# Kernel tuning notes

Measured on AMD Instinct MI355X. Metric: run time of the kernel, lower is better.

Reference implementation:

```python
import jax, jax.numpy as jnp
import numpy as np

B, C, IC, H, W = 2, 64, 32, 96, 96


def setup_inputs() -> dict:
    key = jax.random.key(0)
    ks = jax.random.split(key, 8)
    s_in = 1.0 / np.sqrt(C)
    s_ic = 1.0 / np.sqrt(IC)
    return {
        "x": jax.random.normal(ks[0], (B, C, H, W), dtype=jnp.float32),
        "Wg": jax.random.uniform(ks[1], (IC, C), jnp.float32, -s_in, s_in),
        "bg": jax.random.uniform(ks[2], (IC,), jnp.float32, -s_in, s_in),
        "Wt": jax.random.uniform(ks[3], (IC, C), jnp.float32, -s_in, s_in),
        "bt": jax.random.uniform(ks[4], (IC,), jnp.float32, -s_in, s_in),
        "Wp": jax.random.uniform(ks[5], (IC, C), jnp.float32, -s_in, s_in),
        "bp": jax.random.uniform(ks[6], (IC,), jnp.float32, -s_in, s_in),
        "Wo": jax.random.uniform(ks[7], (C, IC), jnp.float32, -s_ic, s_ic),
        "bo": jax.random.uniform(jax.random.fold_in(key, 9), (C,), jnp.float32, -s_ic, s_ic),
    }


def reference(x, Wg, bg, Wt, bt, Wp, bp, Wo, bo):
    b, c, h, w = x.shape
    n = h * w
    xf = x.reshape(b, c, n)  # [B, C, N]

    def proj(Wc, bc):  # 1x1 conv == channel GEMM -> [B, IC, N]
        return jnp.einsum("bcn,oc->bon", xf, Wc) + bc[None, :, None]

    g = proj(Wg, bg)
    theta = proj(Wt, bt)
    phi = proj(Wp, bp)
    scores = jnp.einsum("bcn,bcm->bnm", theta, phi)  # [B, N, N]
    att = jax.nn.softmax(scores, axis=-1)
    y = jnp.einsum("bnm,bcm->bcn", att, g)  # [B, IC, N]
    o = jnp.einsum("bcn,oc->bon", y, Wo) + bo[None, :, None]  # [B, C, N]
    return o.reshape(b, c, h, w) + x
```

## Files before the change

### kernel.cpp

```cpp
#include <hip/hip_runtime.h>
#include <hip/hip_bf16.h>


#define B_   2
#define C_   64
#define IC_  32
#define N_   9216
#define QBLK128    72
#define LOG2E 1.44269504088896f

typedef __attribute__((ext_vector_type(4))) float  f32x4;
typedef __attribute__((ext_vector_type(8))) short  s16x8;
typedef __attribute__((ext_vector_type(4))) short  s16x4;

static __device__ __forceinline__ ushort f2bf(float f) {
  union { __hip_bfloat16 h; ushort u; } cv;
  cv.h = __float2bfloat16(f);
  return cv.u;
}

static __device__ __forceinline__ float bf2f(ushort u) {
  union { uint i; float f; } c;
  c.i = ((uint)u) << 16;
  return c.f;
}

static __device__ __forceinline__ f32x4 mfma32(s16x8 a, s16x8 b, f32x4 c) {
  return __builtin_amdgcn_mfma_f32_16x16x32_bf16(a, b, c, 0, 0, 0);
}

__global__ __launch_bounds__(256) void proj_kernel(
    const float* __restrict__ x,
    const float* __restrict__ Wg, const float* __restrict__ bg,
    const float* __restrict__ Wt, const float* __restrict__ bt,
    const float* __restrict__ Wp, const float* __restrict__ bp,
    ushort* __restrict__ Qb, ushort* __restrict__ Kb, ushort* __restrict__ Vt)
{
  const int grp = blockIdx.x / 72;
  const int ic0 = grp * 8;
  const int bn  = (blockIdx.x % 72) * 256 + threadIdx.x;
  const int b   = bn / N_;
  const int n   = bn % N_;

  float ag[8], at_[8], ap[8];
#pragma unroll
  for (int j = 0; j < 8; ++j) { ag[j] = 0.f; at_[j] = 0.f; ap[j] = 0.f; }

  const float* xp = x + (size_t)b * C_ * N_ + n;
#pragma unroll 8
  for (int c = 0; c < C_; ++c) {
    const float xv = xp[(size_t)c * N_];
#pragma unroll
    for (int j = 0; j < 8; ++j) {
      ag[j]  = fmaf(Wg[(ic0 + j) * C_ + c], xv, ag[j]);
      at_[j] = fmaf(Wt[(ic0 + j) * C_ + c], xv, at_[j]);
      ap[j]  = fmaf(Wp[(ic0 + j) * C_ + c], xv, ap[j]);
    }
  }

  union { ushort u[8]; s16x8 v; } qv, kv;
#pragma unroll
  for (int j = 0; j < 8; ++j) {
    const int ic = ic0 + j;
    qv.u[j] = f2bf(LOG2E * (at_[j] + bt[ic]));
    kv.u[j] = f2bf(ap[j] + bp[ic]);
  }
  *reinterpret_cast<s16x8*>(Qb + (size_t)bn * IC_ + ic0) = qv.v;
  *reinterpret_cast<s16x8*>(Kb + (size_t)bn * IC_ + ic0) = kv.v;

  const int j6 = n & 63, u = j6 >> 5, r = j6 & 31;
  const int nperm = (n - j6) + u * 32 + (r & 15) * 2 + (r >> 4);
#pragma unroll
  for (int j = 0; j < 8; ++j) {
    const int ic = ic0 + j;
    Vt[(size_t)(b * IC_ + ic) * N_ + nperm] = f2bf(ag[j] + bg[ic]);
  }
}

template<int NSEG>
__global__ __launch_bounds__(256, 4) void attn_kernel(
    const ushort* __restrict__ Qb, const ushort* __restrict__ Kb,
    const ushort* __restrict__ Vt, ushort* __restrict__ Opart,
    float* __restrict__ Lp)
{
  constexpr int NT = 144 / NSEG;
  constexpr int SKEYS = N_ / NSEG;
  constexpr int KSTR = 36;
  constexpr int VSTR = 70;
  __shared__ __align__(16) ushort Kl[64 * KSTR];
  __shared__ __align__(16) ushort Vl[32 * VSTR];

  const int qblk = blockIdx.x % QBLK128;
  const int bs   = blockIdx.x / QBLK128;
  const int seg  = bs % NSEG;
  const int b    = bs / NSEG;
  const int key0 = seg * SKEYS;

  const int tid  = threadIdx.x;
  const int lane = tid & 63;
  const int wave = tid >> 6;
  const int q16  = lane & 15;
  const int h    = lane >> 4;

  const int qbaseA = qblk * 128 + wave * 32;
  const int qbaseB = qbaseA + 16;

  const short ONE = (short)0x3F80;
  const s16x8 ones = {ONE, ONE, ONE, ONE, ONE, ONE, ONE, ONE};

  const s16x8 qfragA = *reinterpret_cast<const s16x8*>(
      Qb + (size_t)(b * N_ + qbaseA + q16) * IC_ + h * 8);
  const s16x8 qfragB = *reinterpret_cast<const s16x8*>(
      Qb + (size_t)(b * N_ + qbaseB + q16) * IC_ + h * 8);

  f32x4 aA0 = {0.f,0.f,0.f,0.f}, aA1 = {0.f,0.f,0.f,0.f}, aLA = {0.f,0.f,0.f,0.f};
  f32x4 aB0 = {0.f,0.f,0.f,0.f}, aB1 = {0.f,0.f,0.f,0.f}, aLB = {0.f,0.f,0.f,0.f};

  const int krow = tid >> 2, kpart = tid & 3;
  const ushort* kg = Kb + ((size_t)b * N_ + key0 + krow) * IC_ + kpart * 8;
  ushort* kl_dst = &Kl[krow * KSTR + kpart * 8];

  const int vd = tid >> 3, vp = tid & 7;
  const ushort* vg = Vt + (size_t)(b * IC_ + vd) * N_ + key0 + vp * 8;
  ushort* vl_dst = &Vl[vd * VSTR + vp * 8];

  s16x8 kreg = *reinterpret_cast<const s16x8*>(kg);
  s16x8 vreg = *reinterpret_cast<const s16x8*>(vg);

  for (int it = 0; it < NT; ++it) {
    *reinterpret_cast<s16x8*>(kl_dst) = kreg;
    *reinterpret_cast<s16x8*>(vl_dst) = vreg;
    __syncthreads();

    if (it + 1 < NT) {
      kg += 64 * IC_;
      vg += 64;
      kreg = *reinterpret_cast<const s16x8*>(kg);
      vreg = *reinterpret_cast<const s16x8*>(vg);
    }

    const s16x8 kf00 = *reinterpret_cast<const s16x8*>(&Kl[(q16)      * KSTR + h * 8]);
    const s16x8 kf01 = *reinterpret_cast<const s16x8*>(&Kl[(16 + q16) * KSTR + h * 8]);
    const s16x8 kf10 = *reinterpret_cast<const s16x8*>(&Kl[(32 + q16) * KSTR + h * 8]);
    const s16x8 kf11 = *reinterpret_cast<const s16x8*>(&Kl[(48 + q16) * KSTR + h * 8]);
    const f32x4 z = {0.f, 0.f, 0.f, 0.f};
    __builtin_amdgcn_s_setprio(1);
    const f32x4 sA0 = mfma32(kf00, qfragA, z);
    const f32x4 sA1 = mfma32(kf01, qfragA, z);
    const f32x4 sB0 = mfma32(kf00, qfragB, z);
    const f32x4 sB1 = mfma32(kf01, qfragB, z);
    const f32x4 sA2 = mfma32(kf10, qfragA, z);
    const f32x4 sA3 = mfma32(kf11, qfragA, z);
    const f32x4 sB2 = mfma32(kf10, qfragB, z);
    const f32x4 sB3 = mfma32(kf11, qfragB, z);
    __builtin_amdgcn_s_setprio(0);

    union { ushort us[8]; s16x8 v; } paA0, paA1, paB0, paB1;
#pragma unroll
    for (int i = 0; i < 4; ++i) {
      paA0.us[2 * i]     = f2bf(__builtin_amdgcn_exp2f(sA0[i]));
      paA0.us[2 * i + 1] = f2bf(__builtin_amdgcn_exp2f(sA1[i]));
      paA1.us[2 * i]     = f2bf(__builtin_amdgcn_exp2f(sA2[i]));
      paA1.us[2 * i + 1] = f2bf(__builtin_amdgcn_exp2f(sA3[i]));
      paB0.us[2 * i]     = f2bf(__builtin_amdgcn_exp2f(sB0[i]));
      paB0.us[2 * i + 1] = f2bf(__builtin_amdgcn_exp2f(sB1[i]));
      paB1.us[2 * i]     = f2bf(__builtin_amdgcn_exp2f(sB2[i]));
      paB1.us[2 * i + 1] = f2bf(__builtin_amdgcn_exp2f(sB3[i]));
    }

    const s16x8 vf00 = *reinterpret_cast<const s16x8*>(&Vl[q16 * VSTR + h * 8]);
    const s16x8 vf01 = *reinterpret_cast<const s16x8*>(&Vl[(16 + q16) * VSTR + h * 8]);
    const s16x8 vf10 = *reinterpret_cast<const s16x8*>(&Vl[q16 * VSTR + 32 + h * 8]);
    const s16x8 vf11 = *reinterpret_cast<const s16x8*>(&Vl[(16 + q16) * VSTR + 32 + h * 8]);
    __builtin_amdgcn_s_setprio(1);
    aA0 = mfma32(paA0.v, vf00, aA0);
    aA1 = mfma32(paA0.v, vf01, aA1);
    aB0 = mfma32(paB0.v, vf00, aB0);
    aB1 = mfma32(paB0.v, vf01, aB1);
    aA0 = mfma32(paA1.v, vf10, aA0);
    aA1 = mfma32(paA1.v, vf11, aA1);
    aB0 = mfma32(paB1.v, vf10, aB0);
    aB1 = mfma32(paB1.v, vf11, aB1);
    aLA = mfma32(paA0.v, ones, aLA);
    aLA = mfma32(paA1.v, ones, aLA);
    aLB = mfma32(paB0.v, ones, aLB);
    aLB = mfma32(paB1.v, ones, aLB);
    __builtin_amdgcn_s_setprio(0);
    __syncthreads();
  }

  const size_t obase0 = ((size_t)(b * NSEG + seg) * N_);
#pragma unroll
  for (int r = 0; r < 4; ++r) {
    const int qA = qbaseA + h * 4 + r;
    const int qB = qbaseB + h * 4 + r;
    Opart[(obase0 + qA) * IC_ + q16]      = f2bf(aA0[r]);
    Opart[(obase0 + qA) * IC_ + 16 + q16] = f2bf(aA1[r]);
    Opart[(obase0 + qB) * IC_ + q16]      = f2bf(aB0[r]);
    Opart[(obase0 + qB) * IC_ + 16 + q16] = f2bf(aB1[r]);
  }
  if (q16 == 0) {
#pragma unroll
    for (int r = 0; r < 4; ++r) {
      Lp[obase0 + qbaseA + h * 4 + r] = aLA[r];
      Lp[obase0 + qbaseB + h * 4 + r] = aLB[r];
    }
  }
}

template<int NSEG>
__global__ __launch_bounds__(256) void combine_kernel(
    const ushort* __restrict__ Opart, const float* __restrict__ Lp,
    ushort* __restrict__ Y)
{
  const int idx = blockIdx.x * 256 + threadIdx.x;
  const int bn  = idx >> 3;
  const int e   = idx & 7;
  const int b   = bn / N_;
  const int q   = bn % N_;

  float l = 0.f;
  float o[4];
#pragma unroll
  for (int j = 0; j < 4; ++j) o[j] = 0.f;

#pragma unroll
  for (int s = 0; s < NSEG; ++s) {
    const size_t base = (size_t)(b * NSEG + s) * N_ + q;
    l += Lp[base];
    union { s16x4 v; ushort us[4]; } ov;
    ov.v = *reinterpret_cast<const s16x4*>(Opart + base * IC_ + e * 4);
#pragma unroll
    for (int j = 0; j < 4; ++j) o[j] += bf2f(ov.us[j]);
  }
  const float inv = 1.0f / l;
  union { ushort us[4]; s16x4 v; } yv;
#pragma unroll
  for (int j = 0; j < 4; ++j) yv.us[j] = f2bf(o[j] * inv);
  *reinterpret_cast<s16x4*>(Y + (size_t)bn * IC_ + e * 4) = yv.v;
}

__global__ __launch_bounds__(256) void out_kernel(
    const ushort* __restrict__ Y, const float* __restrict__ Wo,
    const float* __restrict__ bo, const float* __restrict__ x,
    float* __restrict__ out)
{
  const int g    = blockIdx.x / 72;
  const int oc0  = g * 8;
  const int bn   = (blockIdx.x % 72) * 256 + threadIdx.x;
  const int b    = bn / N_;
  const int n    = bn % N_;

  float yv[32];
#pragma unroll
  for (int i = 0; i < 4; ++i) {
    union { s16x8 v; ushort us[8]; } ov;
    ov.v = *reinterpret_cast<const s16x8*>(Y + (size_t)bn * IC_ + i * 8);
#pragma unroll
    for (int j = 0; j < 8; ++j) yv[i * 8 + j] = bf2f(ov.us[j]);
  }

  float acc[8];
#pragma unroll
  for (int j = 0; j < 8; ++j) acc[j] = bo[oc0 + j];

#pragma unroll
  for (int ic = 0; ic < IC_; ++ic) {
    const float yv_ic = yv[ic];
#pragma unroll
    for (int j = 0; j < 8; ++j)
      acc[j] = fmaf(Wo[(oc0 + j) * IC_ + ic], yv_ic, acc[j]);
  }

#pragma unroll
  for (int j = 0; j < 8; ++j) {
    const int oc = oc0 + j;
    const size_t xi = (size_t)(b * C_ + oc) * N_ + n;
    out[xi] = acc[j] + x[xi];
  }
}

extern "C" void kernel_launch(void* const* d_in, const int* in_sizes, int n_in,
                              void* d_out, int out_size, void* d_ws, size_t ws_size,
                              hipStream_t stream)
{
  const float* x  = (const float*)d_in[0];
  const float* Wg = (const float*)d_in[1];
  const float* bg = (const float*)d_in[2];
  const float* Wt = (const float*)d_in[3];
  const float* bt = (const float*)d_in[4];
  const float* Wp = (const float*)d_in[5];
  const float* bp = (const float*)d_in[6];
  const float* Wo = (const float*)d_in[7];
  const float* bo = (const float*)d_in[8];
  float* out = (float*)d_out;

  char* ws = (char*)d_ws;
  const size_t szb = (size_t)B_ * N_ * IC_ * sizeof(ushort);
  ushort* Qb = (ushort*)(ws);
  ushort* Kb = (ushort*)(ws + szb);
  ushort* Vt = (ushort*)(ws + 2 * szb);
  ushort* Op = (ushort*)(ws + 3 * szb);
  ushort* Yb = (ushort*)(ws);

  const size_t need16 = 3 * szb + 16 * szb + (size_t)16 * B_ * N_ * sizeof(float);

  proj_kernel<<<288, 256, 0, stream>>>(x, Wg, bg, Wt, bt, Wp, bp, Qb, Kb, Vt);
  if (ws_size >= need16) {
    float* Lp = (float*)(ws + 3 * szb + 16 * szb);
    attn_kernel<16><<<B_ * 16 * QBLK128, 256, 0, stream>>>(Qb, Kb, Vt, Op, Lp);
    combine_kernel<16><<<(B_ * N_ * 8) / 256, 256, 0, stream>>>(Op, Lp, Yb);
  } else {
    float* Lp = (float*)(ws + 3 * szb + 8 * szb);
    attn_kernel<8><<<B_ * 8 * QBLK128, 256, 0, stream>>>(Qb, Kb, Vt, Op, Lp);
    combine_kernel<8><<<(B_ * N_ * 8) / 256, 256, 0, stream>>>(Op, Lp, Yb);
  }
  out_kernel<<<8 * 72, 256, 0, stream>>>(Yb, Wo, bo, x, out);
}
```

Baseline: 75.57 us.

## Load K/V fragments directly from global, remap blocks, fuse combine with output projection

The attention kernel drops its LDS staging and both barriers, so each wave loads its K and V MFMA fragments straight from global memory (relying on L2/L1 for reuse across waves and blocks). Block indices are also remapped in an XCD-aware interleaved way so that blocks sharing the same K/V segment land on the same XCD. The separate combine and output-projection kernels are merged into one epilogue kernel, which removes the Y round trip and one launch. The cost is more global/cache traffic per wave, uncoalesced fragment loads, and a heavier per-thread epilogue with 32 accumulators and only 72 blocks.

```diff
diff --git a/kernel.cpp b/kernel.cpp
--- a/kernel.cpp
+++ b/kernel.cpp
@@ -85,13 +85,13 @@
 {
   constexpr int NT = 144 / NSEG;
   constexpr int SKEYS = N_ / NSEG;
-  constexpr int KSTR = 36;
-  constexpr int VSTR = 70;
-  __shared__ __align__(16) ushort Kl[64 * KSTR];
-  __shared__ __align__(16) ushort Vl[32 * VSTR];
-
-  const int qblk = blockIdx.x % QBLK128;
-  const int bs   = blockIdx.x / QBLK128;
+
+  constexpr int NWG = B_ * NSEG * QBLK128;
+  const int bid = blockIdx.x;
+  const int wg  = (bid & 7) * (NWG >> 3) + (bid >> 3);
+
+  const int qblk = wg % QBLK128;
+  const int bs   = wg / QBLK128;
   const int seg  = bs % NSEG;
   const int b    = bs / NSEG;
   const int key0 = seg * SKEYS;
@@ -116,33 +116,21 @@
   f32x4 aA0 = {0.f,0.f,0.f,0.f}, aA1 = {0.f,0.f,0.f,0.f}, aLA = {0.f,0.f,0.f,0.f};
   f32x4 aB0 = {0.f,0.f,0.f,0.f}, aB1 = {0.f,0.f,0.f,0.f}, aLB = {0.f,0.f,0.f,0.f};
 
-  const int krow = tid >> 2, kpart = tid & 3;
-  const ushort* kg = Kb + ((size_t)b * N_ + key0 + krow) * IC_ + kpart * 8;
-  ushort* kl_dst = &Kl[krow * KSTR + kpart * 8];
-
-  const int vd = tid >> 3, vp = tid & 7;
-  const ushort* vg = Vt + (size_t)(b * IC_ + vd) * N_ + key0 + vp * 8;
-  ushort* vl_dst = &Vl[vd * VSTR + vp * 8];
-
-  s16x8 kreg = *reinterpret_cast<const s16x8*>(kg);
-  s16x8 vreg = *reinterpret_cast<const s16x8*>(vg);
+  const ushort* kp  = Kb + ((size_t)b * N_ + key0 + q16) * IC_ + h * 8;
+  const ushort* vp0 = Vt + ((size_t)(b * IC_ + q16)) * N_ + key0 + h * 8;
+  const ushort* vp1 = Vt + ((size_t)(b * IC_ + 16 + q16)) * N_ + key0 + h * 8;
 
   for (int it = 0; it < NT; ++it) {
-    *reinterpret_cast<s16x8*>(kl_dst) = kreg;
-    *reinterpret_cast<s16x8*>(vl_dst) = vreg;
-    __syncthreads();
-
-    if (it + 1 < NT) {
-      kg += 64 * IC_;
-      vg += 64;
-      kreg = *reinterpret_cast<const s16x8*>(kg);
-      vreg = *reinterpret_cast<const s16x8*>(vg);
-    }
-
-    const s16x8 kf00 = *reinterpret_cast<const s16x8*>(&Kl[(q16)      * KSTR + h * 8]);
-    const s16x8 kf01 = *reinterpret_cast<const s16x8*>(&Kl[(16 + q16) * KSTR + h * 8]);
-    const s16x8 kf10 = *reinterpret_cast<const s16x8*>(&Kl[(32 + q16) * KSTR + h * 8]);
-    const s16x8 kf11 = *reinterpret_cast<const s16x8*>(&Kl[(48 + q16) * KSTR + h * 8]);
+    const s16x8 kf00 = *reinterpret_cast<const s16x8*>(kp);
+    const s16x8 kf01 = *reinterpret_cast<const s16x8*>(kp + 16 * IC_);
+    const s16x8 kf10 = *reinterpret_cast<const s16x8*>(kp + 32 * IC_);
+    const s16x8 kf11 = *reinterpret_cast<const s16x8*>(kp + 48 * IC_);
+    const s16x8 vf00 = *reinterpret_cast<const s16x8*>(vp0);
+    const s16x8 vf01 = *reinterpret_cast<const s16x8*>(vp1);
+    const s16x8 vf10 = *reinterpret_cast<const s16x8*>(vp0 + 32);
+    const s16x8 vf11 = *reinterpret_cast<const s16x8*>(vp1 + 32);
+    kp += 64 * IC_; vp0 += 64; vp1 += 64;
+
     const f32x4 z = {0.f, 0.f, 0.f, 0.f};
     __builtin_amdgcn_s_setprio(1);
     const f32x4 sA0 = mfma32(kf00, qfragA, z);
@@ -168,10 +156,6 @@
       paB1.us[2 * i + 1] = f2bf(__builtin_amdgcn_exp2f(sB3[i]));
     }
 
-    const s16x8 vf00 = *reinterpret_cast<const s16x8*>(&Vl[q16 * VSTR + h * 8]);
-    const s16x8 vf01 = *reinterpret_cast<const s16x8*>(&Vl[(16 + q16) * VSTR + h * 8]);
-    const s16x8 vf10 = *reinterpret_cast<const s16x8*>(&Vl[q16 * VSTR + 32 + h * 8]);
-    const s16x8 vf11 = *reinterpret_cast<const s16x8*>(&Vl[(16 + q16) * VSTR + 32 + h * 8]);
     __builtin_amdgcn_s_setprio(1);
     aA0 = mfma32(paA0.v, vf00, aA0);
     aA1 = mfma32(paA0.v, vf01, aA1);
@@ -186,7 +170,6 @@
     aLB = mfma32(paB0.v, ones, aLB);
     aLB = mfma32(paB1.v, ones, aLB);
     __builtin_amdgcn_s_setprio(0);
-    __syncthreads();
   }
 
   const size_t obase0 = ((size_t)(b * NSEG + seg) * N_);
@@ -209,74 +192,53 @@
 }
 
 template<int NSEG>
-__global__ __launch_bounds__(256) void combine_kernel(
+__global__ __launch_bounds__(256) void epilogue_kernel(
     const ushort* __restrict__ Opart, const float* __restrict__ Lp,
-    ushort* __restrict__ Y)
-{
-  const int idx = blockIdx.x * 256 + threadIdx.x;
-  const int bn  = idx >> 3;
-  const int e   = idx & 7;
-  const int b   = bn / N_;
-  const int q   = bn % N_;
+    const float* __restrict__ Wo, const float* __restrict__ bo,
+    const float* __restrict__ x, float* __restrict__ out)
+{
+  const int bn = blockIdx.x * 256 + threadIdx.x;
+  const int b  = bn / N_;
+  const int n  = bn % N_;
 
   float l = 0.f;
-  float o[4];
-#pragma unroll
-  for (int j = 0; j < 4; ++j) o[j] = 0.f;
-
-#pragma unroll
+  float y[32];
+#pragma unroll
+  for (int j = 0; j < 32; ++j) y[j] = 0.f;
+
   for (int s = 0; s < NSEG; ++s) {
-    const size_t base = (size_t)(b * NSEG + s) * N_ + q;
+    const size_t base = (size_t)(b * NSEG + s) * N_ + n;
     l += Lp[base];
-    union { s16x4 v; ushort us[4]; } ov;
-    ov.v = *reinterpret_cast<const s16x4*>(Opart + base * IC_ + e * 4);
-#pragma unroll
-    for (int j = 0; j < 4; ++j) o[j] += bf2f(ov.us[j]);
+#pragma unroll
+    for (int i = 0; i < 4; ++i) {
+      union { s16x8 v; ushort us[8]; } ov;
+      ov.v = *reinterpret_cast<const s16x8*>(Opart + base * IC_ + i * 8);
+#pragma unroll
+      for (int j = 0; j < 8; ++j) y[i * 8 + j] += bf2f(ov.us[j]);
+    }
   }
   const float inv = 1.0f / l;
-  union { ushort us[4]; s16x4 v; } yv;
-#pragma unroll
-  for (int j = 0; j < 4; ++j) yv.us[j] = f2bf(o[j] * inv);
-  *reinterpret_cast<s16x4*>(Y + (size_t)bn * IC_ + e * 4) = yv.v;
-}
-
-__global__ __launch_bounds__(256) void out_kernel(
-    const ushort* __restrict__ Y, const float* __restrict__ Wo,
-    const float* __restrict__ bo, const float* __restrict__ x,
-    float* __restrict__ out)
-{
-  const int g    = blockIdx.x / 72;
-  const int oc0  = g * 8;
-  const int bn   = (blockIdx.x % 72) * 256 + threadIdx.x;
-  const int b    = bn / N_;
-  const int n    = bn % N_;
-
-  float yv[32];
-#pragma unroll
-  for (int i = 0; i < 4; ++i) {
-    union { s16x8 v; ushort us[8]; } ov;
-    ov.v = *reinterpret_cast<const s16x8*>(Y + (size_t)bn * IC_ + i * 8);
-#pragma unroll
-    for (int j = 0; j < 8; ++j) yv[i * 8 + j] = bf2f(ov.us[j]);
-  }
-
-  float acc[8];
-#pragma unroll
-  for (int j = 0; j < 8; ++j) acc[j] = bo[oc0 + j];
-
-#pragma unroll
-  for (int ic = 0; ic < IC_; ++ic) {
-    const float yv_ic = yv[ic];
-#pragma unroll
-    for (int j = 0; j < 8; ++j)
-      acc[j] = fmaf(Wo[(oc0 + j) * IC_ + ic], yv_ic, acc[j]);
-  }
-
-#pragma unroll
-  for (int j = 0; j < 8; ++j) {
-    const int oc = oc0 + j;
-    const size_t xi = (size_t)(b * C_ + oc) * N_ + n;
-    out[xi] = acc[j] + x[xi];
+#pragma unroll
+  for (int j = 0; j < 32; ++j) y[j] *= inv;
+
+#pragma unroll
+  for (int p = 0; p < 4; ++p) {
+    float acc[16];
+#pragma unroll
+    for (int j = 0; j < 16; ++j) acc[j] = bo[p * 16 + j];
+#pragma unroll
+    for (int ic = 0; ic < IC_; ++ic) {
+      const float yv = y[ic];
+#pragma unroll
+      for (int j = 0; j < 16; ++j)
+        acc[j] = fmaf(Wo[(p * 16 + j) * IC_ + ic], yv, acc[j]);
+    }
+#pragma unroll
+    for (int j = 0; j < 16; ++j) {
+      const int oc = p * 16 + j;
+      const size_t xi = (size_t)(b * C_ + oc) * N_ + n;
+      out[xi] = acc[j] + x[xi];
+    }
   }
 }
 
@@ -301,7 +263,6 @@
   ushort* Kb = (ushort*)(ws + szb);
   ushort* Vt = (ushort*)(ws + 2 * szb);
   ushort* Op = (ushort*)(ws + 3 * szb);
-  ushort* Yb = (ushort*)(ws);
 
   const size_t need16 = 3 * szb + 16 * szb + (size_t)16 * B_ * N_ * sizeof(float);
 
@@ -309,11 +270,10 @@
   if (ws_size >= need16) {
     float* Lp = (float*)(ws + 3 * szb + 16 * szb);
     attn_kernel<16><<<B_ * 16 * QBLK128, 256, 0, stream>>>(Qb, Kb, Vt, Op, Lp);
-    combine_kernel<16><<<(B_ * N_ * 8) / 256, 256, 0, stream>>>(Op, Lp, Yb);
+    epilogue_kernel<16><<<(B_ * N_) / 256, 256, 0, stream>>>(Op, Lp, Wo, bo, x, out);
   } else {
     float* Lp = (float*)(ws + 3 * szb + 8 * szb);
     attn_kernel<8><<<B_ * 8 * QBLK128, 256, 0, stream>>>(Qb, Kb, Vt, Op, Lp);
-    combine_kernel<8><<<(B_ * N_ * 8) / 256, 256, 0, stream>>>(Op, Lp, Yb);
-  }
-  out_kernel<<<8 * 72, 256, 0, stream>>>(Yb, Wo, bo, x, out);
-}
+    epilogue_kernel<8><<<(B_ * N_) / 256, 256, 0, stream>>>(Op, Lp, Wo, bo, x, out);
+  }
+}
```

New measurement: 115.5 us. 52.8% more time.

## Widen attention query tile to 64 per wave, add 24-way key split

Applied to the files above, without the earlier changes.

Each wave now handles 64 queries in four 16-row groups instead of 32, so every K/V tile staged in shared memory serves twice as many queries. The loop is restructured to interleave score MFMA, exp and PV MFMA per group, which keeps fewer score registers live at once. A 24-segment key split is added when the workspace is large enough, restoring grid size. The output projection kernel drops to 4 output channels per thread with twice the blocks. The cost is more accumulator registers, which may lower occupancy, and more partial results for the combine step to read.

```diff
diff --git a/kernel.cpp b/kernel.cpp
--- a/kernel.cpp
+++ b/kernel.cpp
@@ -6,7 +6,6 @@
 #define C_   64
 #define IC_  32
 #define N_   9216
-#define QBLK128    72
 #define LOG2E 1.44269504088896f
 
 typedef __attribute__((ext_vector_type(4))) float  f32x4;
@@ -85,13 +84,14 @@
 {
   constexpr int NT = 144 / NSEG;
   constexpr int SKEYS = N_ / NSEG;
+  constexpr int QBLK = N_ / 256;
   constexpr int KSTR = 36;
   constexpr int VSTR = 70;
   __shared__ __align__(16) ushort Kl[64 * KSTR];
   __shared__ __align__(16) ushort Vl[32 * VSTR];
 
-  const int qblk = blockIdx.x % QBLK128;
-  const int bs   = blockIdx.x / QBLK128;
+  const int qblk = blockIdx.x % QBLK;
+  const int bs   = blockIdx.x / QBLK;
   const int seg  = bs % NSEG;
   const int b    = bs / NSEG;
   const int key0 = seg * SKEYS;
@@ -102,27 +102,29 @@
   const int q16  = lane & 15;
   const int h    = lane >> 4;
 
-  const int qbaseA = qblk * 128 + wave * 32;
-  const int qbaseB = qbaseA + 16;
+  const int qbase = qblk * 256 + wave * 64;
 
   const short ONE = (short)0x3F80;
   const s16x8 ones = {ONE, ONE, ONE, ONE, ONE, ONE, ONE, ONE};
 
-  const s16x8 qfragA = *reinterpret_cast<const s16x8*>(
-      Qb + (size_t)(b * N_ + qbaseA + q16) * IC_ + h * 8);
-  const s16x8 qfragB = *reinterpret_cast<const s16x8*>(
-      Qb + (size_t)(b * N_ + qbaseB + q16) * IC_ + h * 8);
+  const ushort* qptr = Qb + (size_t)(b * N_ + qbase + q16) * IC_ + h * 8;
+  const s16x8 qfA = *reinterpret_cast<const s16x8*>(qptr);
+  const s16x8 qfB = *reinterpret_cast<const s16x8*>(qptr + 16 * IC_);
+  const s16x8 qfC = *reinterpret_cast<const s16x8*>(qptr + 32 * IC_);
+  const s16x8 qfD = *reinterpret_cast<const s16x8*>(qptr + 48 * IC_);
 
   f32x4 aA0 = {0.f,0.f,0.f,0.f}, aA1 = {0.f,0.f,0.f,0.f}, aLA = {0.f,0.f,0.f,0.f};
   f32x4 aB0 = {0.f,0.f,0.f,0.f}, aB1 = {0.f,0.f,0.f,0.f}, aLB = {0.f,0.f,0.f,0.f};
+  f32x4 aC0 = {0.f,0.f,0.f,0.f}, aC1 = {0.f,0.f,0.f,0.f}, aLC = {0.f,0.f,0.f,0.f};
+  f32x4 aD0 = {0.f,0.f,0.f,0.f}, aD1 = {0.f,0.f,0.f,0.f}, aLD = {0.f,0.f,0.f,0.f};
 
   const int krow = tid >> 2, kpart = tid & 3;
   const ushort* kg = Kb + ((size_t)b * N_ + key0 + krow) * IC_ + kpart * 8;
   ushort* kl_dst = &Kl[krow * KSTR + kpart * 8];
 
-  const int vd = tid >> 3, vp = tid & 7;
-  const ushort* vg = Vt + (size_t)(b * IC_ + vd) * N_ + key0 + vp * 8;
-  ushort* vl_dst = &Vl[vd * VSTR + vp * 8];
+  const int vd = tid >> 3, vpp = tid & 7;
+  const ushort* vg = Vt + (size_t)(b * IC_ + vd) * N_ + key0 + vpp * 8;
+  ushort* vl_dst = &Vl[vd * VSTR + vpp * 8];
 
   s16x8 kreg = *reinterpret_cast<const s16x8*>(kg);
   s16x8 vreg = *reinterpret_cast<const s16x8*>(vg);
@@ -139,71 +141,106 @@
       vreg = *reinterpret_cast<const s16x8*>(vg);
     }
 
-    const s16x8 kf00 = *reinterpret_cast<const s16x8*>(&Kl[(q16)      * KSTR + h * 8]);
-    const s16x8 kf01 = *reinterpret_cast<const s16x8*>(&Kl[(16 + q16) * KSTR + h * 8]);
-    const s16x8 kf10 = *reinterpret_cast<const s16x8*>(&Kl[(32 + q16) * KSTR + h * 8]);
-    const s16x8 kf11 = *reinterpret_cast<const s16x8*>(&Kl[(48 + q16) * KSTR + h * 8]);
-    const f32x4 z = {0.f, 0.f, 0.f, 0.f};
-    __builtin_amdgcn_s_setprio(1);
-    const f32x4 sA0 = mfma32(kf00, qfragA, z);
-    const f32x4 sA1 = mfma32(kf01, qfragA, z);
-    const f32x4 sB0 = mfma32(kf00, qfragB, z);
-    const f32x4 sB1 = mfma32(kf01, qfragB, z);
-    const f32x4 sA2 = mfma32(kf10, qfragA, z);
-    const f32x4 sA3 = mfma32(kf11, qfragA, z);
-    const f32x4 sB2 = mfma32(kf10, qfragB, z);
-    const f32x4 sB3 = mfma32(kf11, qfragB, z);
-    __builtin_amdgcn_s_setprio(0);
-
-    union { ushort us[8]; s16x8 v; } paA0, paA1, paB0, paB1;
-#pragma unroll
-    for (int i = 0; i < 4; ++i) {
-      paA0.us[2 * i]     = f2bf(__builtin_amdgcn_exp2f(sA0[i]));
-      paA0.us[2 * i + 1] = f2bf(__builtin_amdgcn_exp2f(sA1[i]));
-      paA1.us[2 * i]     = f2bf(__builtin_amdgcn_exp2f(sA2[i]));
-      paA1.us[2 * i + 1] = f2bf(__builtin_amdgcn_exp2f(sA3[i]));
-      paB0.us[2 * i]     = f2bf(__builtin_amdgcn_exp2f(sB0[i]));
-      paB0.us[2 * i + 1] = f2bf(__builtin_amdgcn_exp2f(sB1[i]));
-      paB1.us[2 * i]     = f2bf(__builtin_amdgcn_exp2f(sB2[i]));
-      paB1.us[2 * i + 1] = f2bf(__builtin_amdgcn_exp2f(sB3[i]));
+#pragma unroll
+    for (int u = 0; u < 2; ++u) {
+      const s16x8 kf0 = *reinterpret_cast<const s16x8*>(&Kl[(u * 32 + q16) * KSTR + h * 8]);
+      const s16x8 kf1 = *reinterpret_cast<const s16x8*>(&Kl[(u * 32 + 16 + q16) * KSTR + h * 8]);
+      const s16x8 vf0 = *reinterpret_cast<const s16x8*>(&Vl[q16 * VSTR + u * 32 + h * 8]);
+      const s16x8 vf1 = *reinterpret_cast<const s16x8*>(&Vl[(16 + q16) * VSTR + u * 32 + h * 8]);
+      const f32x4 z = {0.f, 0.f, 0.f, 0.f};
+
+      {
+        __builtin_amdgcn_s_setprio(1);
+        const f32x4 s0 = mfma32(kf0, qfA, z);
+        const f32x4 s1 = mfma32(kf1, qfA, z);
+        __builtin_amdgcn_s_setprio(0);
+        union { ushort us[8]; s16x8 v; } pa;
+#pragma unroll
+        for (int i = 0; i < 4; ++i) {
+          pa.us[2 * i]     = f2bf(__builtin_amdgcn_exp2f(s0[i]));
+          pa.us[2 * i + 1] = f2bf(__builtin_amdgcn_exp2f(s1[i]));
+        }
+        __builtin_amdgcn_s_setprio(1);
+        aA0 = mfma32(pa.v, vf0, aA0);
+        aA1 = mfma32(pa.v, vf1, aA1);
+        aLA = mfma32(pa.v, ones, aLA);
+        __builtin_amdgcn_s_setprio(0);
+      }
+      {
+        __builtin_amdgcn_s_setprio(1);
+        const f32x4 s0 = mfma32(kf0, qfB, z);
+        const f32x4 s1 = mfma32(kf1, qfB, z);
+        __builtin_amdgcn_s_setprio(0);
+        union { ushort us[8]; s16x8 v; } pa;
+#pragma unroll
+        for (int i = 0; i < 4; ++i) {
+          pa.us[2 * i]     = f2bf(__builtin_amdgcn_exp2f(s0[i]));
+          pa.us[2 * i + 1] = f2bf(__builtin_amdgcn_exp2f(s1[i]));
+        }
+        __builtin_amdgcn_s_setprio(1);
+        aB0 = mfma32(pa.v, vf0, aB0);
+        aB1 = mfma32(pa.v, vf1, aB1);
+        aLB = mfma32(pa.v, ones, aLB);
+        __builtin_amdgcn_s_setprio(0);
+      }
+      {
+        __builtin_amdgcn_s_setprio(1);
+        const f32x4 s0 = mfma32(kf0, qfC, z);
+        const f32x4 s1 = mfma32(kf1, qfC, z);
+        __builtin_amdgcn_s_setprio(0);
+        union { ushort us[8]; s16x8 v; } pa;
+#pragma unroll
+        for (int i = 0; i < 4; ++i) {
+          pa.us[2 * i]     = f2bf(__builtin_amdgcn_exp2f(s0[i]));
+          pa.us[2 * i + 1] = f2bf(__builtin_amdgcn_exp2f(s1[i]));
+        }
+        __builtin_amdgcn_s_setprio(1);
+        aC0 = mfma32(pa.v, vf0, aC0);
+        aC1 = mfma32(pa.v, vf1, aC1);
+        aLC = mfma32(pa.v, ones, aLC);
+        __builtin_amdgcn_s_setprio(0);
+      }
+      {
+        __builtin_amdgcn_s_setprio(1);
+        const f32x4 s0 = mfma32(kf0, qfD, z);
+        const f32x4 s1 = mfma32(kf1, qfD, z);
+        __builtin_amdgcn_s_setprio(0);
+        union { ushort us[8]; s16x8 v; } pa;
+#pragma unroll
+        for (int i = 0; i < 4; ++i) {
+          pa.us[2 * i]     = f2bf(__builtin_amdgcn_exp2f(s0[i]));
+          pa.us[2 * i + 1] = f2bf(__builtin_amdgcn_exp2f(s1[i]));
+        }
+        __builtin_amdgcn_s_setprio(1);
+        aD0 = mfma32(pa.v, vf0, aD0);
+        aD1 = mfma32(pa.v, vf1, aD1);
+        aLD = mfma32(pa.v, ones, aLD);
+        __builtin_amdgcn_s_setprio(0);
+      }
     }
-
-    const s16x8 vf00 = *reinterpret_cast<const s16x8*>(&Vl[q16 * VSTR + h * 8]);
-    const s16x8 vf01 = *reinterpret_cast<const s16x8*>(&Vl[(16 + q16) * VSTR + h * 8]);
-    const s16x8 vf10 = *reinterpret_cast<const s16x8*>(&Vl[q16 * VSTR + 32 + h * 8]);
-    const s16x8 vf11 = *reinterpret_cast<const s16x8*>(&Vl[(16 + q16) * VSTR + 32 + h * 8]);
-    __builtin_amdgcn_s_setprio(1);
-    aA0 = mfma32(paA0.v, vf00, aA0);
-    aA1 = mfma32(paA0.v, vf01, aA1);
-    aB0 = mfma32(paB0.v, vf00, aB0);
-    aB1 = mfma32(paB0.v, vf01, aB1);
-    aA0 = mfma32(paA1.v, vf10, aA0);
-    aA1 = mfma32(paA1.v, vf11, aA1);
-    aB0 = mfma32(paB1.v, vf10, aB0);
-    aB1 = mfma32(paB1.v, vf11, aB1);
-    aLA = mfma32(paA0.v, ones, aLA);
-    aLA = mfma32(paA1.v, ones, aLA);
-    aLB = mfma32(paB0.v, ones, aLB);
-    aLB = mfma32(paB1.v, ones, aLB);
-    __builtin_amdgcn_s_setprio(0);
     __syncthreads();
   }
 
   const size_t obase0 = ((size_t)(b * NSEG + seg) * N_);
 #pragma unroll
   for (int r = 0; r < 4; ++r) {
-    const int qA = qbaseA + h * 4 + r;
-    const int qB = qbaseB + h * 4 + r;
-    Opart[(obase0 + qA) * IC_ + q16]      = f2bf(aA0[r]);
-    Opart[(obase0 + qA) * IC_ + 16 + q16] = f2bf(aA1[r]);
-    Opart[(obase0 + qB) * IC_ + q16]      = f2bf(aB0[r]);
-    Opart[(obase0 + qB) * IC_ + 16 + q16] = f2bf(aB1[r]);
+    const int qA = qbase + h * 4 + r;
+    Opart[(obase0 + qA) * IC_ + q16]           = f2bf(aA0[r]);
+    Opart[(obase0 + qA) * IC_ + 16 + q16]      = f2bf(aA1[r]);
+    Opart[(obase0 + qA + 16) * IC_ + q16]      = f2bf(aB0[r]);
+    Opart[(obase0 + qA + 16) * IC_ + 16 + q16] = f2bf(aB1[r]);
+    Opart[(obase0 + qA + 32) * IC_ + q16]      = f2bf(aC0[r]);
+    Opart[(obase0 + qA + 32) * IC_ + 16 + q16] = f2bf(aC1[r]);
+    Opart[(obase0 + qA + 48) * IC_ + q16]      = f2bf(aD0[r]);
+    Opart[(obase0 + qA + 48) * IC_ + 16 + q16] = f2bf(aD1[r]);
   }
   if (q16 == 0) {
 #pragma unroll
     for (int r = 0; r < 4; ++r) {
-      Lp[obase0 + qbaseA + h * 4 + r] = aLA[r];
-      Lp[obase0 + qbaseB + h * 4 + r] = aLB[r];
+      Lp[obase0 + qbase + h * 4 + r]      = aLA[r];
+      Lp[obase0 + qbase + 16 + h * 4 + r] = aLB[r];
+      Lp[obase0 + qbase + 32 + h * 4 + r] = aLC[r];
+      Lp[obase0 + qbase + 48 + h * 4 + r] = aLD[r];
     }
   }
 }
@@ -246,7 +283,7 @@
     float* __restrict__ out)
 {
   const int g    = blockIdx.x / 72;
-  const int oc0  = g * 8;
+  const int oc0  = g * 4;
   const int bn   = (blockIdx.x % 72) * 256 + threadIdx.x;
   const int b    = bn / N_;
   const int n    = bn % N_;
@@ -260,20 +297,20 @@
     for (int j = 0; j < 8; ++j) yv[i * 8 + j] = bf2f(ov.us[j]);
   }
 
-  float acc[8];
-#pragma unroll
-  for (int j = 0; j < 8; ++j) acc[j] = bo[oc0 + j];
+  float acc[4];
+#pragma unroll
+  for (int j = 0; j < 4; ++j) acc[j] = bo[oc0 + j];
 
 #pragma unroll
   for (int ic = 0; ic < IC_; ++ic) {
     const float yv_ic = yv[ic];
 #pragma unroll
-    for (int j = 0; j < 8; ++j)
+    for (int j = 0; j < 4; ++j)
       acc[j] = fmaf(Wo[(oc0 + j) * IC_ + ic], yv_ic, acc[j]);
   }
 
 #pragma unroll
-  for (int j = 0; j < 8; ++j) {
+  for (int j = 0; j < 4; ++j) {
     const int oc = oc0 + j;
     const size_t xi = (size_t)(b * C_ + oc) * N_ + n;
     out[xi] = acc[j] + x[xi];
@@ -303,17 +340,22 @@
   ushort* Op = (ushort*)(ws + 3 * szb);
   ushort* Yb = (ushort*)(ws);
 
+  const size_t need24 = 3 * szb + 24 * szb + (size_t)24 * B_ * N_ * sizeof(float);
   const size_t need16 = 3 * szb + 16 * szb + (size_t)16 * B_ * N_ * sizeof(float);
 
   proj_kernel<<<288, 256, 0, stream>>>(x, Wg, bg, Wt, bt, Wp, bp, Qb, Kb, Vt);
-  if (ws_size >= need16) {
+  if (ws_size >= need24) {
+    float* Lp = (float*)(ws + 3 * szb + 24 * szb);
+    attn_kernel<24><<<B_ * 24 * (N_ / 256), 256, 0, stream>>>(Qb, Kb, Vt, Op, Lp);
+    combine_kernel<24><<<(B_ * N_ * 8) / 256, 256, 0, stream>>>(Op, Lp, Yb);
+  } else if (ws_size >= need16) {
     float* Lp = (float*)(ws + 3 * szb + 16 * szb);
-    attn_kernel<16><<<B_ * 16 * QBLK128, 256, 0, stream>>>(Qb, Kb, Vt, Op, Lp);
+    attn_kernel<16><<<B_ * 16 * (N_ / 256), 256, 0, stream>>>(Qb, Kb, Vt, Op, Lp);
     combine_kernel<16><<<(B_ * N_ * 8) / 256, 256, 0, stream>>>(Op, Lp, Yb);
   } else {
     float* Lp = (float*)(ws + 3 * szb + 8 * szb);
-    attn_kernel<8><<<B_ * 8 * QBLK128, 256, 0, stream>>>(Qb, Kb, Vt, Op, Lp);
+    attn_kernel<8><<<B_ * 8 * (N_ / 256), 256, 0, stream>>>(Qb, Kb, Vt, Op, Lp);
     combine_kernel<8><<<(B_ * N_ * 8) / 256, 256, 0, stream>>>(Op, Lp, Yb);
   }
-  out_kernel<<<8 * 72, 256, 0, stream>>>(Yb, Wo, bo, x, out);
-}
+  out_kernel<<<16 * 72, 256, 0, stream>>>(Yb, Wo, bo, x, out);
+}
```

Measured after the change: 69.78 us. 7.7% less time.

## Fuse split-KV combine with output projection and raise attention occupancy bound

Applied to the files above, without the earlier changes.

Merges the combine kernel (summing partial attention outputs and normalising) with the output 1x1 projection plus residual into one epilogue kernel. Normalised rows are staged in LDS, so the Y buffer no longer makes a bf16 round trip through global memory and one launch is removed. Also raises the attention kernel's launch_bounds min-blocks from 4 to 8, which pressures the compiler to cap registers per thread and may cause spills. The epilogue uses 32 positions per block, so each block does one x/out store per channel strip, which may coalesce less well than before.

```diff
diff --git a/kernel.cpp b/kernel.cpp
--- a/kernel.cpp
+++ b/kernel.cpp
@@ -6,7 +6,7 @@
 #define C_   64
 #define IC_  32
 #define N_   9216
-#define QBLK128    72
+#define QBLK128 72
 #define LOG2E 1.44269504088896f
 
 typedef __attribute__((ext_vector_type(4))) float  f32x4;
@@ -78,7 +78,7 @@
 }
 
 template<int NSEG>
-__global__ __launch_bounds__(256, 4) void attn_kernel(
+__global__ __launch_bounds__(256, 8) void attn_kernel(
     const ushort* __restrict__ Qb, const ushort* __restrict__ Kb,
     const ushort* __restrict__ Vt, ushort* __restrict__ Opart,
     float* __restrict__ Lp)
@@ -120,9 +120,9 @@
   const ushort* kg = Kb + ((size_t)b * N_ + key0 + krow) * IC_ + kpart * 8;
   ushort* kl_dst = &Kl[krow * KSTR + kpart * 8];
 
-  const int vd = tid >> 3, vp = tid & 7;
-  const ushort* vg = Vt + (size_t)(b * IC_ + vd) * N_ + key0 + vp * 8;
-  ushort* vl_dst = &Vl[vd * VSTR + vp * 8];
+  const int vd = tid >> 3, vpp = tid & 7;
+  const ushort* vg = Vt + (size_t)(b * IC_ + vd) * N_ + key0 + vpp * 8;
+  ushort* vl_dst = &Vl[vd * VSTR + vpp * 8];
 
   s16x8 kreg = *reinterpret_cast<const s16x8*>(kg);
   s16x8 vreg = *reinterpret_cast<const s16x8*>(vg);
@@ -209,74 +209,66 @@
 }
 
 template<int NSEG>
-__global__ __launch_bounds__(256) void combine_kernel(
+__global__ __launch_bounds__(256) void epilogue_kernel(
     const ushort* __restrict__ Opart, const float* __restrict__ Lp,
-    ushort* __restrict__ Y)
+    const float* __restrict__ Wo, const float* __restrict__ bo,
+    const float* __restrict__ x, float* __restrict__ out)
 {
-  const int idx = blockIdx.x * 256 + threadIdx.x;
-  const int bn  = idx >> 3;
-  const int e   = idx & 7;
-  const int b   = bn / N_;
-  const int q   = bn % N_;
-
-  float l = 0.f;
-  float o[4];
-#pragma unroll
-  for (int j = 0; j < 4; ++j) o[j] = 0.f;
-
-#pragma unroll
-  for (int s = 0; s < NSEG; ++s) {
-    const size_t base = (size_t)(b * NSEG + s) * N_ + q;
-    l += Lp[base];
-    union { s16x4 v; ushort us[4]; } ov;
-    ov.v = *reinterpret_cast<const s16x4*>(Opart + base * IC_ + e * 4);
-#pragma unroll
-    for (int j = 0; j < 4; ++j) o[j] += bf2f(ov.us[j]);
-  }
-  const float inv = 1.0f / l;
-  union { ushort us[4]; s16x4 v; } yv;
-#pragma unroll
-  for (int j = 0; j < 4; ++j) yv.us[j] = f2bf(o[j] * inv);
-  *reinterpret_cast<s16x4*>(Y + (size_t)bn * IC_ + e * 4) = yv.v;
-}
-
-__global__ __launch_bounds__(256) void out_kernel(
-    const ushort* __restrict__ Y, const float* __restrict__ Wo,
-    const float* __restrict__ bo, const float* __restrict__ x,
-    float* __restrict__ out)
-{
-  const int g    = blockIdx.x / 72;
-  const int oc0  = g * 8;
-  const int bn   = (blockIdx.x % 72) * 256 + threadIdx.x;
-  const int b    = bn / N_;
-  const int n    = bn % N_;
-
-  float yv[32];
-#pragma unroll
-  for (int i = 0; i < 4; ++i) {
-    union { s16x8 v; ushort us[8]; } ov;
-    ov.v = *reinterpret_cast<const s16x8*>(Y + (size_t)bn * IC_ + i * 8);
-#pragma unroll
-    for (int j = 0; j < 8; ++j) yv[i * 8 + j] = bf2f(ov.us[j]);
-  }
-
-  float acc[8];
-#pragma unroll
-  for (int j = 0; j < 8; ++j) acc[j] = bo[oc0 + j];
-
-#pragma unroll
-  for (int ic = 0; ic < IC_; ++ic) {
-    const float yv_ic = yv[ic];
-#pragma unroll
-    for (int j = 0; j < 8; ++j)
-      acc[j] = fmaf(Wo[(oc0 + j) * IC_ + ic], yv_ic, acc[j]);
-  }
-
-#pragma unroll
-  for (int j = 0; j < 8; ++j) {
-    const int oc = oc0 + j;
-    const size_t xi = (size_t)(b * C_ + oc) * N_ + n;
-    out[xi] = acc[j] + x[xi];
+  __shared__ float ylds[32][33];
+
+  const int tid = threadIdx.x;
+  const int bn0 = blockIdx.x * 32;
+
+  {
+    const int p  = tid >> 3;
+    const int e  = tid & 7;
+    const int bn = bn0 + p;
+    const int b  = bn / N_;
+    const int q  = bn % N_;
+
+    float l = 0.f;
+    float o[4] = {0.f, 0.f, 0.f, 0.f};
+#pragma unroll
+    for (int s = 0; s < NSEG; ++s) {
+      const size_t base = (size_t)(b * NSEG + s) * N_ + q;
+      l += Lp[base];
+      union { s16x4 v; ushort us[4]; } ov;
+      ov.v = *reinterpret_cast<const s16x4*>(Opart + base * IC_ + e * 4);
+#pragma unroll
+      for (int j = 0; j < 4; ++j) o[j] += bf2f(ov.us[j]);
+    }
+    const float inv = 1.0f / l;
+#pragma unroll
+    for (int j = 0; j < 4; ++j) ylds[p][e * 4 + j] = o[j] * inv;
+  }
+  __syncthreads();
+
+  {
+    const int pe  = tid & 31;
+    const int g   = tid >> 5;
+    const int oc0 = g * 8;
+    const int bn  = bn0 + pe;
+    const int b   = bn / N_;
+    const int n   = bn % N_;
+
+    float acc[8];
+#pragma unroll
+    for (int j = 0; j < 8; ++j) acc[j] = bo[oc0 + j];
+
+#pragma unroll
+    for (int ic = 0; ic < IC_; ++ic) {
+      const float yv = ylds[pe][ic];
+#pragma unroll
+      for (int j = 0; j < 8; ++j)
+        acc[j] = fmaf(Wo[(oc0 + j) * IC_ + ic], yv, acc[j]);
+    }
+
+#pragma unroll
+    for (int j = 0; j < 8; ++j) {
+      const int oc = oc0 + j;
+      const size_t xi = (size_t)(b * C_ + oc) * N_ + n;
+      out[xi] = acc[j] + x[xi];
+    }
   }
 }
 
@@ -301,19 +293,19 @@
   ushort* Kb = (ushort*)(ws + szb);
   ushort* Vt = (ushort*)(ws + 2 * szb);
   ushort* Op = (ushort*)(ws + 3 * szb);
-  ushort* Yb = (ushort*)(ws);
 
   const size_t need16 = 3 * szb + 16 * szb + (size_t)16 * B_ * N_ * sizeof(float);
+  const size_t need8  = 3 * szb + 8 * szb + (size_t)8 * B_ * N_ * sizeof(float);
+  const int epiblocks = (B_ * N_) / 32;
 
   proj_kernel<<<288, 256, 0, stream>>>(x, Wg, bg, Wt, bt, Wp, bp, Qb, Kb, Vt);
   if (ws_size >= need16) {
     float* Lp = (float*)(ws + 3 * szb + 16 * szb);
     attn_kernel<16><<<B_ * 16 * QBLK128, 256, 0, stream>>>(Qb, Kb, Vt, Op, Lp);
-    combine_kernel<16><<<(B_ * N_ * 8) / 256, 256, 0, stream>>>(Op, Lp, Yb);
+    epilogue_kernel<16><<<epiblocks, 256, 0, stream>>>(Op, Lp, Wo, bo, x, out);
   } else {
     float* Lp = (float*)(ws + 3 * szb + 8 * szb);
     attn_kernel<8><<<B_ * 8 * QBLK128, 256, 0, stream>>>(Qb, Kb, Vt, Op, Lp);
-    combine_kernel<8><<<(B_ * N_ * 8) / 256, 256, 0, stream>>>(Op, Lp, Yb);
-  }
-  out_kernel<<<8 * 72, 256, 0, stream>>>(Yb, Wo, bo, x, out);
-}
+    epilogue_kernel<8><<<epiblocks, 256, 0, stream>>>(Op, Lp, Wo, bo, x, out);
+  }
+}
```

After: 211.4 us. +179.7%, slower.
